# Kernel tuning notes

Hardware: AMD Instinct MI355X
Metric: run time of the kernel (lower is better)

The kernel has to match this reference:

```python
import jax, jax.numpy as jnp
import numpy as np

N, E = 100000, 1000000
IN_F, HID, OUT, K = 64, 64, 32, 3


def setup_inputs() -> dict:
    key = jax.random.key(0)
    ks = jax.random.split(key, 8)
    s = 0.05
    return {
        "features": jax.random.normal(ks[0], (N, IN_F), dtype=jnp.float32),
        "src": jax.random.randint(ks[1], (E,), 0, N),
        "dst": jax.random.randint(ks[2], (E,), 0, N),
        "n_nodes": N,
        "W1": jax.random.normal(ks[3], (K * IN_F, HID), jnp.float32) * s,
        "b1": jnp.zeros((HID,), jnp.float32),
        "W2": jax.random.normal(ks[4], (K * HID, HID), jnp.float32) * s,
        "b2": jnp.zeros((HID,), jnp.float32),
        "Wm1": jax.random.normal(ks[5], (HID, HID), jnp.float32) * s,
        "bm1": jnp.zeros((HID,), jnp.float32),
        "Wm2": jax.random.normal(ks[6], (HID, OUT), jnp.float32) * s,
        "bm2": jnp.zeros((OUT,), jnp.float32),
    }


def _cheb_conv(x, src, dst, dinv, W, b, n_nodes, k=K):
    # DGL ChebConv with lambda_max = 2 (re_norm = 2/lambda_max = 1).
    def prop(h):  # D^{-1/2} A D^{-1/2} h via edge gather/scatter
        m = (h * dinv)[src]                                   # [E, F]
        agg = jax.ops.segment_sum(m, dst, num_segments=n_nodes)
        return agg * dinv

    X0 = x
    Xs = [X0]
    X1 = -prop(X0)                 # -re_norm*L h + (re_norm-1)*X0, re_norm=1
    Xs.append(X1)
    for _ in range(2, k):
        Xi = -2.0 * prop(X1) - X0  # Chebyshev recursion
        Xs.append(Xi)
        X0, X1 = X1, Xi
    return jnp.concatenate(Xs, axis=1) @ W + b  # Linear(k*F_in -> F_out)


def reference(features, src, dst, n_nodes, W1, b1, W2, b2, Wm1, bm1, Wm2, bm2):
    deg = jax.ops.segment_sum(
        jnp.ones((src.shape[0],), dtype=features.dtype), dst, num_segments=n_nodes
    )
    dinv = (jnp.clip(deg, 1.0, None) ** -0.5)[:, None]  # in-degree^{-1/2}
    x = jax.nn.relu(_cheb_conv(features, src, dst, dinv, W1, b1, n_nodes))
    x = jax.nn.relu(_cheb_conv(x, src, dst, dinv, W2, b2, n_nodes))
    return jax.nn.relu(x @ Wm1 + bm1) @ Wm2 + bm2
```

## Files before the change

kernel.cpp:

```cpp
#include <hip/hip_runtime.h>


typedef unsigned short ushort_t;
typedef __attribute__((ext_vector_type(8))) short v8s;
typedef __attribute__((ext_vector_type(4))) float v4f;

__device__ inline ushort_t f2bf(float f) {
    unsigned u = __float_as_uint(f);
    return (ushort_t)((u + 0x7FFFu + ((u >> 16) & 1u)) >> 16);
}
__device__ inline float bf2f(ushort_t h) {
    return __uint_as_float(((unsigned)h) << 16);
}

#define BSH 9
#define BSZ (1 << BSH)
#define CHUNK 4096


__global__ __launch_bounds__(256) void k_bhist(const int* __restrict__ dst,
                                               int* __restrict__ gbase, int E, int NB) {
    __shared__ int h[1024];
    for (int i = threadIdx.x; i < NB; i += 256) h[i] = 0;
    __syncthreads();
    for (int i = blockIdx.x * blockDim.x + threadIdx.x; i < E; i += gridDim.x * blockDim.x)
        atomicAdd(&h[dst[i] >> BSH], 1);
    __syncthreads();
    for (int i = threadIdx.x; i < NB; i += 256)
        if (h[i]) atomicAdd(&gbase[i], h[i]);
}

__global__ void k_bscan(int* __restrict__ gbase, int* __restrict__ gcur, int NB) {
    __shared__ int sh[1024];
    int t = threadIdx.x;
    int v = (t < NB) ? gbase[t] : 0;
    sh[t] = v;
    __syncthreads();
    for (int off = 1; off < 1024; off <<= 1) {
        int u = 0;
        if (t >= off) u = sh[t - off];
        __syncthreads();
        sh[t] += u;
        __syncthreads();
    }
    if (t < NB) {
        int excl = sh[t] - v;
        gbase[t] = excl;
        gcur[t] = excl;
    }
}

__global__ __launch_bounds__(256) void k_bucket2(
    const int* __restrict__ src, const int* __restrict__ dst,
    int* __restrict__ gcur, int2* __restrict__ eb, int E, int NB) {
    __shared__ int ls[CHUNK];
    __shared__ int ld[CHUNK];
    __shared__ int hist[1024];
    __shared__ int bbase[1024];
    int t = threadIdx.x;
    int base = blockIdx.x * CHUNK;
    int count = E - base;
    if (count > CHUNK) count = CHUNK;
    for (int i = t; i < NB; i += 256) hist[i] = 0;
    __syncthreads();
    for (int i = t; i < count; i += 256) {
        int s = src[base + i];
        int d = dst[base + i];
        ls[i] = s;
        ld[i] = d;
        atomicAdd(&hist[d >> BSH], 1);
    }
    __syncthreads();
    for (int b = t; b < NB; b += 256) {
        int c = hist[b];
        bbase[b] = c ? atomicAdd(&gcur[b], c) : 0;
        hist[b] = 0;
    }
    __syncthreads();
    for (int i = t; i < count; i += 256) {
        int d = ld[i];
        int b = d >> BSH;
        int off = atomicAdd(&hist[b], 1);
        eb[bbase[b] + off] = make_int2(ls[i], d);
    }
}

__global__ __launch_bounds__(256) void k_local(
    const int2* __restrict__ eb, const int* __restrict__ gbase,
    int* __restrict__ col, int* __restrict__ row_ptr,
    float* __restrict__ dinv, int N, int E, int NB) {
    __shared__ int cnt[BSZ];
    __shared__ int tsum[256];
    int t = threadIdx.x;
    int b = blockIdx.x;
    int d0 = b << BSH;
    cnt[2 * t] = 0;
    cnt[2 * t + 1] = 0;
    __syncthreads();
    int beg = gbase[b];
    int end = (b + 1 < NB) ? gbase[b + 1] : E;
    for (int i = beg + t; i < end; i += 256)
        atomicAdd(&cnt[eb[i].y - d0], 1);
    __syncthreads();
    int c0 = cnt[2 * t], c1 = cnt[2 * t + 1];
    int mysum = c0 + c1;
    tsum[t] = mysum;
    __syncthreads();
    for (int off = 1; off < 256; off <<= 1) {
        int u = 0;
        if (t >= off) u = tsum[t - off];
        __syncthreads();
        tsum[t] += u;
        __syncthreads();
    }
    int rbase = beg + tsum[t] - mysum;
    int d = d0 + 2 * t;
    if (d < N) {
        row_ptr[d] = rbase;
        dinv[d] = rsqrtf(fmaxf((float)c0, 1.0f));
    }
    if (d + 1 < N) {
        row_ptr[d + 1] = rbase + c0;
        dinv[d + 1] = rsqrtf(fmaxf((float)c1, 1.0f));
    }
    cnt[2 * t] = rbase;
    cnt[2 * t + 1] = rbase + c0;
    __syncthreads();
    for (int i = beg + t; i < end; i += 256) {
        int2 e = eb[i];
        int p = atomicAdd(&cnt[e.y - d0], 1);
        col[p] = e.x;
    }
    if (b == NB - 1 && t == 0) row_ptr[N] = E;
}

__global__ void k_wprep(const float* __restrict__ W1, const float* __restrict__ W2,
                        const float* __restrict__ Wm1, const float* __restrict__ Wm2,
                        ushort_t* __restrict__ W1t, ushort_t* __restrict__ W2t,
                        ushort_t* __restrict__ Wm1t, ushort_t* __restrict__ Wm2t) {
    int i = blockIdx.x * 256 + threadIdx.x;
    if (i < 12288) { int k = i >> 6, n = i & 63; W1t[n * 192 + k] = f2bf(W1[i]); return; }
    i -= 12288;
    if (i < 12288) { int k = i >> 6, n = i & 63; W2t[n * 192 + k] = f2bf(W2[i]); return; }
    i -= 12288;
    if (i < 4096) { int k = i >> 6, n = i & 63; Wm1t[n * 64 + k] = f2bf(Wm1[i]); return; }
    i -= 4096;
    if (i < 2048) { int k = i >> 5, n = i & 31; Wm2t[n * 64 + k] = f2bf(Wm2[i]); }
}

__global__ void k_tobf16(const float4* __restrict__ X, const float* __restrict__ dinv,
                         ushort4* __restrict__ Y, int n4) {
    int i = blockIdx.x * blockDim.x + threadIdx.x;
    if (i < n4) {
        float s = dinv[i >> 4];
        float4 v = X[i];
        ushort4 o;
        o.x = f2bf(v.x * s); o.y = f2bf(v.y * s); o.z = f2bf(v.z * s); o.w = f2bf(v.w * s);
        Y[i] = o;
    }
}

template <int MODE>
__global__ __launch_bounds__(256) void k_prop(
    const ushort_t* __restrict__ Xb, const int* __restrict__ rp,
    const int* __restrict__ col, const float* __restrict__ dinv,
    const ushort_t* __restrict__ X0b, ushort_t* __restrict__ OUTB, int N) {
    int wid = (blockIdx.x * blockDim.x + threadIdx.x) >> 6;
    int lane = threadIdx.x & 63;
    if (wid >= N) return;
    int g = lane >> 4;
    int fl = (lane & 15) * 4;
    int beg = rp[wid], end = rp[wid + 1];
    float4 a0 = make_float4(0.f, 0.f, 0.f, 0.f);
    float4 a1 = make_float4(0.f, 0.f, 0.f, 0.f);
    int e = beg + g;
    for (; e + 4 < end; e += 8) {
        int s0 = col[e], s1 = col[e + 4];
        ushort4 u0 = *(const ushort4*)&Xb[(size_t)s0 * 64 + fl];
        ushort4 u1 = *(const ushort4*)&Xb[(size_t)s1 * 64 + fl];
        a0.x += bf2f(u0.x); a0.y += bf2f(u0.y); a0.z += bf2f(u0.z); a0.w += bf2f(u0.w);
        a1.x += bf2f(u1.x); a1.y += bf2f(u1.y); a1.z += bf2f(u1.z); a1.w += bf2f(u1.w);
    }
    if (e < end) {
        int s0 = col[e];
        ushort4 u0 = *(const ushort4*)&Xb[(size_t)s0 * 64 + fl];
        a0.x += bf2f(u0.x); a0.y += bf2f(u0.y); a0.z += bf2f(u0.z); a0.w += bf2f(u0.w);
    }
    float4 acc;
    acc.x = a0.x + a1.x;
    acc.y = a0.y + a1.y;
    acc.z = a0.z + a1.z;
    acc.w = a0.w + a1.w;
    acc.x += __shfl_xor(acc.x, 16);
    acc.y += __shfl_xor(acc.y, 16);
    acc.z += __shfl_xor(acc.z, 16);
    acc.w += __shfl_xor(acc.w, 16);
    acc.x += __shfl_xor(acc.x, 32);
    acc.y += __shfl_xor(acc.y, 32);
    acc.z += __shfl_xor(acc.z, 32);
    acc.w += __shfl_xor(acc.w, 32);
    if (g == 0) {
        float di = dinv[wid];
        float4 o;
        if (MODE == 1) {
            float m = -di * di;
            o.x = m * acc.x; o.y = m * acc.y; o.z = m * acc.z; o.w = m * acc.w;
        } else {
            ushort4 x0u = *(const ushort4*)&X0b[(size_t)wid * 64 + fl];
            float m = -2.0f * di;
            float rd = 1.0f / di;
            o.x = fmaf(m, acc.x, -rd * bf2f(x0u.x));
            o.y = fmaf(m, acc.y, -rd * bf2f(x0u.y));
            o.z = fmaf(m, acc.z, -rd * bf2f(x0u.z));
            o.w = fmaf(m, acc.w, -rd * bf2f(x0u.w));
        }
        ushort4 ob;
        ob.x = f2bf(o.x); ob.y = f2bf(o.y); ob.z = f2bf(o.z); ob.w = f2bf(o.w);
        *(ushort4*)&OUTB[(size_t)wid * 64 + fl] = ob;
    }
}

template <bool SCALE_OUT>
__global__ __launch_bounds__(256) void k_cheb_mfma(
    const ushort_t* __restrict__ X0, const ushort_t* __restrict__ X1,
    const ushort_t* __restrict__ X2, const float* __restrict__ dinv,
    const ushort_t* __restrict__ Wt,
    const float* __restrict__ b, ushort_t* __restrict__ Yb, int N) {
    int wave = threadIdx.x >> 6, lane = threadIdx.x & 63;
    int n16 = lane & 15, q = lane >> 4;
    int node0 = blockIdx.x * 64;
    int arow = node0 + wave * 16 + n16;
    const ushort_t* Xc[3] = {X0, X1, X2};

    v4f acc_s[4], acc_u[4];
#pragma unroll
    for (int t = 0; t < 4; t++) {
        acc_s[t] = (v4f){0.f, 0.f, 0.f, 0.f};
        acc_u[t] = (v4f){0.f, 0.f, 0.f, 0.f};
    }

#pragma unroll
    for (int ks = 0; ks < 6; ks++) {
        int c = ks >> 1;
        int kk = (ks & 1) * 32 + q * 8;
        v8s av = {0, 0, 0, 0, 0, 0, 0, 0};
        if (arow < N) av = *(const v8s*)&Xc[c][(size_t)arow * 64 + kk];
#pragma unroll
        for (int t = 0; t < 4; t++) {
            v8s bv = *(const v8s*)&Wt[(size_t)(t * 16 + n16) * 192 + ks * 32 + q * 8];
            if (c < 2)
                acc_s[t] = __builtin_amdgcn_mfma_f32_16x16x32_bf16(av, bv, acc_s[t], 0, 0, 0);
            else
                acc_u[t] = __builtin_amdgcn_mfma_f32_16x16x32_bf16(av, bv, acc_u[t], 0, 0, 0);
        }
    }

    int rbase = node0 + wave * 16 + q * 4;
#pragma unroll
    for (int r = 0; r < 4; r++) {
        int row = rbase + r;
        if (row < N) {
            float dv = dinv[row];
            float rd = 1.0f / dv;
            float s = SCALE_OUT ? dv : 1.0f;
#pragma unroll
            for (int t = 0; t < 4; t++) {
                float y = fmaf(rd, acc_s[t][r], acc_u[t][r]) + b[t * 16 + n16];
                y = fmaxf(y, 0.0f);
                Yb[(size_t)row * 64 + t * 16 + n16] = f2bf(s * y);
            }
        }
    }
}

__global__ __launch_bounds__(256) void k_mlp_mfma(
    const ushort_t* __restrict__ Hb, const ushort_t* __restrict__ W1t,
    const float* __restrict__ b1, const ushort_t* __restrict__ W2t,
    const float* __restrict__ b2, float* __restrict__ out, int N) {
    __shared__ ushort_t Hs[64][76];
    int wave = threadIdx.x >> 6, lane = threadIdx.x & 63;
    int n16 = lane & 15, q = lane >> 4;
    int node0 = blockIdx.x * 64;
    int arow = node0 + wave * 16 + n16;

    v4f acc[4];
#pragma unroll
    for (int t = 0; t < 4; t++) acc[t] = (v4f){0.f, 0.f, 0.f, 0.f};
#pragma unroll
    for (int ks = 0; ks < 2; ks++) {
        v8s av = {0, 0, 0, 0, 0, 0, 0, 0};
        if (arow < N) av = *(const v8s*)&Hb[(size_t)arow * 64 + ks * 32 + q * 8];
#pragma unroll
        for (int t = 0; t < 4; t++) {
            v8s bv = *(const v8s*)&W1t[(size_t)(t * 16 + n16) * 64 + ks * 32 + q * 8];
            acc[t] = __builtin_amdgcn_mfma_f32_16x16x32_bf16(av, bv, acc[t], 0, 0, 0);
        }
    }
    int lr = wave * 16 + q * 4;
#pragma unroll
    for (int r = 0; r < 4; r++)
#pragma unroll
        for (int t = 0; t < 4; t++) {
            float y = acc[t][r] + b1[t * 16 + n16];
            Hs[lr + r][t * 16 + n16] = f2bf(fmaxf(y, 0.0f));
        }
    __syncthreads();

    v4f a2[2];
    a2[0] = (v4f){0.f, 0.f, 0.f, 0.f};
    a2[1] = (v4f){0.f, 0.f, 0.f, 0.f};
#pragma unroll
    for (int ks = 0; ks < 2; ks++) {
        v8s av = *(const v8s*)&Hs[wave * 16 + n16][ks * 32 + q * 8];
#pragma unroll
        for (int t = 0; t < 2; t++) {
            v8s bv = *(const v8s*)&W2t[(size_t)(t * 16 + n16) * 64 + ks * 32 + q * 8];
            a2[t] = __builtin_amdgcn_mfma_f32_16x16x32_bf16(av, bv, a2[t], 0, 0, 0);
        }
    }
    int rbase = node0 + wave * 16 + q * 4;
#pragma unroll
    for (int r = 0; r < 4; r++) {
        int row = rbase + r;
        if (row < N) {
#pragma unroll
            for (int t = 0; t < 2; t++)
                out[(size_t)row * 32 + t * 16 + n16] = a2[t][r] + b2[t * 16 + n16];
        }
    }
}

extern "C" void kernel_launch(void* const* d_in, const int* in_sizes, int n_in,
                              void* d_out, int out_size, void* d_ws, size_t ws_size,
                              hipStream_t stream) {
    const float* features = (const float*)d_in[0];
    const int* src = (const int*)d_in[1];
    const int* dst = (const int*)d_in[2];
    const float* W1 = (const float*)d_in[4];
    const float* b1 = (const float*)d_in[5];
    const float* W2 = (const float*)d_in[6];
    const float* b2 = (const float*)d_in[7];
    const float* Wm1 = (const float*)d_in[8];
    const float* bm1 = (const float*)d_in[9];
    const float* Wm2 = (const float*)d_in[10];
    const float* bm2 = (const float*)d_in[11];
    float* out = (float*)d_out;

    int N = in_sizes[0] / 64;
    int E = in_sizes[1];
    int NB = (N + BSZ - 1) >> BSH;

    float* ws = (float*)d_ws;
    float* dinv = ws;
    int* row_ptr = (int*)(dinv + N);
    int* gbase = row_ptr + (N + 1);
    int* gcur = gbase + 1024;
    int* col = gcur + 1024;
    int2* eb = (int2*)(((uintptr_t)(col + E) + 7) & ~(uintptr_t)7);
    ushort_t* Fb  = (ushort_t*)(eb + E);
    ushort_t* X1b = Fb  + (size_t)N * 64;
    ushort_t* X2b = X1b + (size_t)N * 64;
    ushort_t* H1b = X2b + (size_t)N * 64;
    ushort_t* H2b = H1b + (size_t)N * 64;
    ushort_t* W1t = H2b + (size_t)N * 64;
    ushort_t* W2t = W1t + 64 * 192;
    ushort_t* Wm1t = W2t + 64 * 192;
    ushort_t* Wm2t = Wm1t + 64 * 64;

    int pblk = (N * 64 + 255) / 256;
    int gblk = (N + 63) / 64;
    int n4 = N * 16;
    int cblk = (n4 + 255) / 256;
    int bblk = (E + CHUNK - 1) / CHUNK;

    k_wprep<<<(30720 + 255) / 256, 256, 0, stream>>>(W1, W2, Wm1, Wm2, W1t, W2t, Wm1t, Wm2t);

    hipMemsetAsync(gbase, 0, NB * sizeof(int), stream);
    k_bhist<<<512, 256, 0, stream>>>(dst, gbase, E, NB);
    k_bscan<<<1, 1024, 0, stream>>>(gbase, gcur, NB);
    k_bucket2<<<bblk, 256, 0, stream>>>(src, dst, gcur, eb, E, NB);
    k_local<<<NB, 256, 0, stream>>>(eb, gbase, col, row_ptr, dinv, N, E, NB);

    k_tobf16<<<cblk, 256, 0, stream>>>((const float4*)features, dinv, (ushort4*)Fb, n4);

    k_prop<1><<<pblk, 256, 0, stream>>>(Fb, row_ptr, col, dinv, nullptr, X1b, N);
    k_prop<2><<<pblk, 256, 0, stream>>>(X1b, row_ptr, col, dinv, Fb, X2b, N);
    k_cheb_mfma<true><<<gblk, 256, 0, stream>>>(Fb, X1b, X2b, dinv, W1t, b1, H1b, N);

    k_prop<1><<<pblk, 256, 0, stream>>>(H1b, row_ptr, col, dinv, nullptr, X1b, N);
    k_prop<2><<<pblk, 256, 0, stream>>>(X1b, row_ptr, col, dinv, H1b, X2b, N);
    k_cheb_mfma<false><<<gblk, 256, 0, stream>>>(H1b, X1b, X2b, dinv, W2t, b2, H2b, N);

    k_mlp_mfma<<<gblk, 256, 0, stream>>>(H2b, Wm1t, bm1, Wm2t, bm2, out, N);
}
```

Baseline: 395.9 us.

## Fuse bucket scan into histogram, pack edges, widen prop loads to 16 bytes

Several changes land together. The bucket histogram and scan are merged into one kernel, with a last-block-done counter in place of a separate scan launch. Bucketed edges are packed into a single int (src<<9 | local dst) with a byte-sized bucket id in LDS, which halves edge-buffer traffic. k_local caches up to 24 edges per thread in registers so it does not reread them. k_prop switches to 8 lanes per row with 16-byte bf16 loads and 8 edge groups. The packing assumes NB ≤ 256 and src < 2^22, which holds for N=100000 but not in general.

```diff
diff --git a/kernel.cpp b/kernel.cpp
--- a/kernel.cpp
+++ b/kernel.cpp
@@ -3,6 +3,7 @@
 
 typedef unsigned short ushort_t;
 typedef __attribute__((ext_vector_type(8))) short v8s;
+typedef __attribute__((ext_vector_type(8))) unsigned short u8s;
 typedef __attribute__((ext_vector_type(4))) float v4f;
 
 __device__ inline ushort_t f2bf(float f) {
@@ -17,34 +18,35 @@
 #define BSZ (1 << BSH)
 #define CHUNK 4096
 
-
-__global__ __launch_bounds__(256) void k_bhist(const int* __restrict__ dst,
-                                               int* __restrict__ gbase, int E, int NB) {
-    __shared__ int h[1024];
-    for (int i = threadIdx.x; i < NB; i += 256) h[i] = 0;
-    __syncthreads();
-    for (int i = blockIdx.x * blockDim.x + threadIdx.x; i < E; i += gridDim.x * blockDim.x)
+__global__ __launch_bounds__(256) void k_bhist(
+    const int* __restrict__ dst, int* __restrict__ gbase, int* __restrict__ gcur,
+    int* __restrict__ done, int E, int NB) {
+    __shared__ int h[256];
+    __shared__ int sc[256];
+    __shared__ int isLast;
+    int t = threadIdx.x;
+    h[t] = 0;
+    __syncthreads();
+    for (int i = blockIdx.x * 256 + t; i < E; i += gridDim.x * 256)
         atomicAdd(&h[dst[i] >> BSH], 1);
     __syncthreads();
-    for (int i = threadIdx.x; i < NB; i += 256)
-        if (h[i]) atomicAdd(&gbase[i], h[i]);
-}
-
-__global__ void k_bscan(int* __restrict__ gbase, int* __restrict__ gcur, int NB) {
-    __shared__ int sh[1024];
-    int t = threadIdx.x;
-    int v = (t < NB) ? gbase[t] : 0;
-    sh[t] = v;
-    __syncthreads();
-    for (int off = 1; off < 1024; off <<= 1) {
+    if (t < NB && h[t]) atomicAdd(&gbase[t], h[t]);
+    __threadfence();
+    if (t == 0) isLast = (atomicAdd(done, 1) == (int)gridDim.x - 1);
+    __syncthreads();
+    if (!isLast) return;
+    int v = (t < NB) ? atomicAdd(&gbase[t], 0) : 0;
+    sc[t] = v;
+    __syncthreads();
+    for (int off = 1; off < 256; off <<= 1) {
         int u = 0;
-        if (t >= off) u = sh[t - off];
+        if (t >= off) u = sc[t - off];
         __syncthreads();
-        sh[t] += u;
+        sc[t] += u;
         __syncthreads();
     }
     if (t < NB) {
-        int excl = sh[t] - v;
+        int excl = sc[t] - v;
         gbase[t] = excl;
         gcur[t] = excl;
     }
@@ -52,41 +54,41 @@
 
 __global__ __launch_bounds__(256) void k_bucket2(
     const int* __restrict__ src, const int* __restrict__ dst,
-    int* __restrict__ gcur, int2* __restrict__ eb, int E, int NB) {
-    __shared__ int ls[CHUNK];
-    __shared__ int ld[CHUNK];
-    __shared__ int hist[1024];
-    __shared__ int bbase[1024];
+    int* __restrict__ gcur, int* __restrict__ eb, int E, int NB) {
+    __shared__ int lv[CHUNK];
+    __shared__ unsigned char lb[CHUNK];
+    __shared__ int hist[256];
+    __shared__ int bbase[256];
     int t = threadIdx.x;
     int base = blockIdx.x * CHUNK;
     int count = E - base;
     if (count > CHUNK) count = CHUNK;
-    for (int i = t; i < NB; i += 256) hist[i] = 0;
+    hist[t] = 0;
     __syncthreads();
     for (int i = t; i < count; i += 256) {
         int s = src[base + i];
         int d = dst[base + i];
-        ls[i] = s;
-        ld[i] = d;
-        atomicAdd(&hist[d >> BSH], 1);
-    }
-    __syncthreads();
-    for (int b = t; b < NB; b += 256) {
-        int c = hist[b];
-        bbase[b] = c ? atomicAdd(&gcur[b], c) : 0;
-        hist[b] = 0;
+        int b = d >> BSH;
+        lv[i] = (s << BSH) | (d & (BSZ - 1));
+        lb[i] = (unsigned char)b;
+        atomicAdd(&hist[b], 1);
+    }
+    __syncthreads();
+    {
+        int c = hist[t];
+        bbase[t] = (t < NB && c) ? atomicAdd(&gcur[t], c) : 0;
+        hist[t] = 0;
     }
     __syncthreads();
     for (int i = t; i < count; i += 256) {
-        int d = ld[i];
-        int b = d >> BSH;
+        int b = lb[i];
         int off = atomicAdd(&hist[b], 1);
-        eb[bbase[b] + off] = make_int2(ls[i], d);
+        eb[bbase[b] + off] = lv[i];
     }
 }
 
 __global__ __launch_bounds__(256) void k_local(
-    const int2* __restrict__ eb, const int* __restrict__ gbase,
+    const int* __restrict__ eb, const int* __restrict__ gbase,
     int* __restrict__ col, int* __restrict__ row_ptr,
     float* __restrict__ dinv, int N, int E, int NB) {
     __shared__ int cnt[BSZ];
@@ -99,8 +101,15 @@
     __syncthreads();
     int beg = gbase[b];
     int end = (b + 1 < NB) ? gbase[b + 1] : E;
-    for (int i = beg + t; i < end; i += 256)
-        atomicAdd(&cnt[eb[i].y - d0], 1);
+    int le[24];
+    {
+        int k = 0;
+        for (int i = beg + t; i < end; i += 256, k++) {
+            int v = eb[i];
+            if (k < 24) le[k] = v;
+            atomicAdd(&cnt[v & (BSZ - 1)], 1);
+        }
+    }
     __syncthreads();
     int c0 = cnt[2 * t], c1 = cnt[2 * t + 1];
     int mysum = c0 + c1;
@@ -126,10 +135,13 @@
     cnt[2 * t] = rbase;
     cnt[2 * t + 1] = rbase + c0;
     __syncthreads();
-    for (int i = beg + t; i < end; i += 256) {
-        int2 e = eb[i];
-        int p = atomicAdd(&cnt[e.y - d0], 1);
-        col[p] = e.x;
+    {
+        int k = 0;
+        for (int i = beg + t; i < end; i += 256, k++) {
+            int v = (k < 24) ? le[k] : eb[i];
+            int p = atomicAdd(&cnt[v & (BSZ - 1)], 1);
+            col[p] = v >> BSH;
+        }
     }
     if (b == NB - 1 && t == 0) row_ptr[N] = E;
 }
@@ -168,55 +180,50 @@
     int wid = (blockIdx.x * blockDim.x + threadIdx.x) >> 6;
     int lane = threadIdx.x & 63;
     if (wid >= N) return;
-    int g = lane >> 4;
-    int fl = (lane & 15) * 4;
+    int g = lane >> 3;
+    int fl = (lane & 7) * 8;
     int beg = rp[wid], end = rp[wid + 1];
-    float4 a0 = make_float4(0.f, 0.f, 0.f, 0.f);
-    float4 a1 = make_float4(0.f, 0.f, 0.f, 0.f);
+    float a0[8] = {0, 0, 0, 0, 0, 0, 0, 0};
+    float a1[8] = {0, 0, 0, 0, 0, 0, 0, 0};
     int e = beg + g;
-    for (; e + 4 < end; e += 8) {
-        int s0 = col[e], s1 = col[e + 4];
-        ushort4 u0 = *(const ushort4*)&Xb[(size_t)s0 * 64 + fl];
-        ushort4 u1 = *(const ushort4*)&Xb[(size_t)s1 * 64 + fl];
-        a0.x += bf2f(u0.x); a0.y += bf2f(u0.y); a0.z += bf2f(u0.z); a0.w += bf2f(u0.w);
-        a1.x += bf2f(u1.x); a1.y += bf2f(u1.y); a1.z += bf2f(u1.z); a1.w += bf2f(u1.w);
+    for (; e + 8 < end; e += 16) {
+        int s0 = col[e], s1 = col[e + 8];
+        u8s u0 = *(const u8s*)&Xb[(size_t)s0 * 64 + fl];
+        u8s u1 = *(const u8s*)&Xb[(size_t)s1 * 64 + fl];
+#pragma unroll
+        for (int j = 0; j < 8; j++) a0[j] += bf2f(u0[j]);
+#pragma unroll
+        for (int j = 0; j < 8; j++) a1[j] += bf2f(u1[j]);
     }
     if (e < end) {
         int s0 = col[e];
-        ushort4 u0 = *(const ushort4*)&Xb[(size_t)s0 * 64 + fl];
-        a0.x += bf2f(u0.x); a0.y += bf2f(u0.y); a0.z += bf2f(u0.z); a0.w += bf2f(u0.w);
-    }
-    float4 acc;
-    acc.x = a0.x + a1.x;
-    acc.y = a0.y + a1.y;
-    acc.z = a0.z + a1.z;
-    acc.w = a0.w + a1.w;
-    acc.x += __shfl_xor(acc.x, 16);
-    acc.y += __shfl_xor(acc.y, 16);
-    acc.z += __shfl_xor(acc.z, 16);
-    acc.w += __shfl_xor(acc.w, 16);
-    acc.x += __shfl_xor(acc.x, 32);
-    acc.y += __shfl_xor(acc.y, 32);
-    acc.z += __shfl_xor(acc.z, 32);
-    acc.w += __shfl_xor(acc.w, 32);
+        u8s u0 = *(const u8s*)&Xb[(size_t)s0 * 64 + fl];
+#pragma unroll
+        for (int j = 0; j < 8; j++) a0[j] += bf2f(u0[j]);
+    }
+    float acc[8];
+#pragma unroll
+    for (int j = 0; j < 8; j++) acc[j] = a0[j] + a1[j];
+#pragma unroll
+    for (int st = 8; st < 64; st <<= 1)
+#pragma unroll
+        for (int j = 0; j < 8; j++) acc[j] += __shfl_xor(acc[j], st);
     if (g == 0) {
         float di = dinv[wid];
-        float4 o;
+        u8s ob;
         if (MODE == 1) {
             float m = -di * di;
-            o.x = m * acc.x; o.y = m * acc.y; o.z = m * acc.z; o.w = m * acc.w;
+#pragma unroll
+            for (int j = 0; j < 8; j++) ob[j] = f2bf(m * acc[j]);
         } else {
-            ushort4 x0u = *(const ushort4*)&X0b[(size_t)wid * 64 + fl];
+            u8s x0u = *(const u8s*)&X0b[(size_t)wid * 64 + fl];
             float m = -2.0f * di;
             float rd = 1.0f / di;
-            o.x = fmaf(m, acc.x, -rd * bf2f(x0u.x));
-            o.y = fmaf(m, acc.y, -rd * bf2f(x0u.y));
-            o.z = fmaf(m, acc.z, -rd * bf2f(x0u.z));
-            o.w = fmaf(m, acc.w, -rd * bf2f(x0u.w));
-        }
-        ushort4 ob;
-        ob.x = f2bf(o.x); ob.y = f2bf(o.y); ob.z = f2bf(o.z); ob.w = f2bf(o.w);
-        *(ushort4*)&OUTB[(size_t)wid * 64 + fl] = ob;
+#pragma unroll
+            for (int j = 0; j < 8; j++)
+                ob[j] = f2bf(fmaf(m, acc[j], -rd * bf2f(x0u[j])));
+        }
+        *(u8s*)&OUTB[(size_t)wid * 64 + fl] = ob;
     }
 }
 
@@ -224,8 +231,8 @@
 __global__ __launch_bounds__(256) void k_cheb_mfma(
     const ushort_t* __restrict__ X0, const ushort_t* __restrict__ X1,
     const ushort_t* __restrict__ X2, const float* __restrict__ dinv,
-    const ushort_t* __restrict__ Wt,
-    const float* __restrict__ b, ushort_t* __restrict__ Yb, int N) {
+    const ushort_t* __restrict__ Wt, const float* __restrict__ b,
+    ushort_t* __restrict__ Yb, int N) {
     int wave = threadIdx.x >> 6, lane = threadIdx.x & 63;
     int n16 = lane & 15, q = lane >> 4;
     int node0 = blockIdx.x * 64;
@@ -238,7 +245,6 @@
         acc_s[t] = (v4f){0.f, 0.f, 0.f, 0.f};
         acc_u[t] = (v4f){0.f, 0.f, 0.f, 0.f};
     }
-
 #pragma unroll
     for (int ks = 0; ks < 6; ks++) {
         int c = ks >> 1;
@@ -254,7 +260,6 @@
                 acc_u[t] = __builtin_amdgcn_mfma_f32_16x16x32_bf16(av, bv, acc_u[t], 0, 0, 0);
         }
     }
-
     int rbase = node0 + wave * 16 + q * 4;
 #pragma unroll
     for (int r = 0; r < 4; r++) {
@@ -354,9 +359,10 @@
     float* dinv = ws;
     int* row_ptr = (int*)(dinv + N);
     int* gbase = row_ptr + (N + 1);
-    int* gcur = gbase + 1024;
-    int* col = gcur + 1024;
-    int2* eb = (int2*)(((uintptr_t)(col + E) + 7) & ~(uintptr_t)7);
+    int* gcur = gbase + 256;
+    int* done = gcur + 256;
+    int* col = done + 1;
+    int* eb = col + E;
     ushort_t* Fb  = (ushort_t*)(eb + E);
     ushort_t* X1b = Fb  + (size_t)N * 64;
     ushort_t* X2b = X1b + (size_t)N * 64;
@@ -374,10 +380,9 @@
     int bblk = (E + CHUNK - 1) / CHUNK;
 
     k_wprep<<<(30720 + 255) / 256, 256, 0, stream>>>(W1, W2, Wm1, Wm2, W1t, W2t, Wm1t, Wm2t);
-
-    hipMemsetAsync(gbase, 0, NB * sizeof(int), stream);
-    k_bhist<<<512, 256, 0, stream>>>(dst, gbase, E, NB);
-    k_bscan<<<1, 1024, 0, stream>>>(gbase, gcur, NB);
+    hipMemsetAsync(gbase, 0, 513 * sizeof(int), stream);
+
+    k_bhist<<<256, 256, 0, stream>>>(dst, gbase, gcur, done, E, NB);
     k_bucket2<<<bblk, 256, 0, stream>>>(src, dst, gcur, eb, E, NB);
     k_local<<<NB, 256, 0, stream>>>(eb, gbase, col, row_ptr, dinv, N, E, NB);
 
```

New measurement: 407.6 us. +3.0%, slower.
